# Kernel optimization log

Hardware: AMD Instinct MI355X
Metric: run time of the kernel (lower is better)

Reference implementation:

```python
import jax, jax.numpy as jnp
import numpy as np

B, N, D_SIM = 4096, 64, 768
NLI_DIM = 768
KK = 5
H1, NUM_CLASSES = 1024, 4


def setup_inputs() -> dict:
    key = jax.random.key(0)
    ks = jax.random.split(key, 8)
    sim_stance_emb = jax.random.normal(ks[0], (B, D_SIM), dtype=jnp.float32)
    nli_stance_emb = jax.random.normal(ks[1], (B, NLI_DIM), dtype=jnp.float32)
    sim_body_emb = jax.random.normal(ks[2], (B, N, D_SIM), dtype=jnp.float32)
    nli_body_emb = jax.random.normal(ks[3], (B, N, NLI_DIM), dtype=jnp.float32)
    fan1 = (KK + 1) * NLI_DIM
    W1 = jax.random.uniform(ks[4], (H1, fan1), jnp.float32, -1.0, 1.0) / jnp.sqrt(fan1)
    b1 = jax.random.uniform(ks[5], (H1,), jnp.float32, -1.0, 1.0) / jnp.sqrt(fan1)
    W2 = jax.random.uniform(ks[6], (NUM_CLASSES, H1), jnp.float32, -1.0, 1.0) / jnp.sqrt(H1)
    b2 = jax.random.uniform(ks[7], (NUM_CLASSES,), jnp.float32, -1.0, 1.0) / jnp.sqrt(H1)
    return {"sim_stance_emb": sim_stance_emb, "nli_stance_emb": nli_stance_emb,
            "sim_body_emb": sim_body_emb, "nli_body_emb": nli_body_emb,
            "W1": W1, "b1": b1, "W2": W2, "b2": b2}


def reference(sim_stance_emb, nli_stance_emb, sim_body_emb, nli_body_emb, W1, b1, W2, b2):
    # sims[b, n] = <sim_stance_emb[b], sim_body_emb[b, n]>  (bmm + squeeze)
    sims = jnp.einsum('bd,bnd->bn', sim_stance_emb, sim_body_emb)
    _, top_idx = jax.lax.top_k(sims, KK)                      # [B, KK]
    # gather top-k nli body sentence embeddings: [B, KK, NLI_DIM]
    top_emb = jnp.take_along_axis(nli_body_emb, top_idx[:, :, None], axis=1)
    xx = jnp.concatenate([nli_stance_emb, top_emb.reshape(top_emb.shape[0], -1)], axis=1)
    xx = jax.nn.relu(xx @ W1.T + b1)
    return xx @ W2.T + b2
```

## Files before the change

kernel.cpp:

```cpp
#include <hip/hip_runtime.h>
#include <stdint.h>
#include <stddef.h>

#define B_N   4096
#define NSENT 64
#define DDIM  768
#define TOPK  5
#define FAN1  4608
#define H1DIM 1024
#define NCLS  4
#define KDIM  4608

typedef __attribute__((ext_vector_type(8))) __bf16 bf16x8;
typedef __attribute__((ext_vector_type(4))) float  f32x4;

__device__ __forceinline__ unsigned short f2bf(float f) {
    unsigned int u = __float_as_uint(f);
    unsigned int r = (u + 0x7fffu + ((u >> 16) & 1u)) >> 16;
    return (unsigned short)r;
}

__device__ __forceinline__ void gl_lds16(const void* g, void* l) {
    __builtin_amdgcn_global_load_lds((__attribute__((address_space(1))) void*)(g),
                                     (__attribute__((address_space(3))) void*)(l),
                                     16, 0, 0);
}

__global__ __launch_bounds__(256) void k_topk_gather(
    const float* __restrict__ sim_stance,
    const float* __restrict__ sim_body,
    const float* __restrict__ nli_stance,
    const float* __restrict__ nli_body,
    unsigned short* __restrict__ xx)
{
    const int b    = blockIdx.x;
    const int tid  = threadIdx.x;
    const int lane = tid & 63;
    const int wave = tid >> 6;
    const int g    = lane >> 4;
    const int c    = lane & 15;
    __shared__ float sims[NSENT];
    __shared__ int   topidx[TOPK];

    const float4* st4 = (const float4*)(sim_stance + (size_t)b * DDIM);
    float4 st[12];
    #pragma unroll
    for (int j = 0; j < 12; ++j) st[j] = st4[c + 16 * j];

    const float* bodyb = sim_body + (size_t)b * NSENT * DDIM;
    #pragma unroll 1
    for (int it = 0; it < 4; ++it) {
        const int r = wave * 16 + it * 4 + g;
        const float4* r4 = (const float4*)(bodyb + (size_t)r * DDIM);
        float p = 0.f;
        #pragma unroll
        for (int j = 0; j < 12; ++j) {
            float4 v = r4[c + 16 * j];
            p += v.x*st[j].x + v.y*st[j].y + v.z*st[j].z + v.w*st[j].w;
        }
        #pragma unroll
        for (int off = 8; off; off >>= 1) p += __shfl_xor(p, off);
        if (c == 0) sims[r] = p;
    }
    __syncthreads();

    if (wave == 0) {
        float v = sims[lane];
        #pragma unroll
        for (int k = 0; k < TOPK; ++k) {
            float bv = v; int bi = lane;
            #pragma unroll
            for (int off = 32; off; off >>= 1) {
                float ov = __shfl_xor(bv, off);
                int   oi = __shfl_xor(bi, off);
                if (ov > bv || (ov == bv && oi < bi)) { bv = ov; bi = oi; }
            }
            if (lane == 0) topidx[k] = bi;
            if (lane == bi) v = -3.402823466e38f;
        }
    }
    __syncthreads();

    unsigned short* xrow = xx + (size_t)b * FAN1;
    for (int task = tid; task < 1152; task += 256) {
        const int seg = task / 192;
        const int t   = task - seg * 192;
        const float* src = (seg == 0)
            ? (nli_stance + (size_t)b * DDIM)
            : (nli_body + ((size_t)b * NSENT + topidx[seg - 1]) * DDIM);
        float4 v = ((const float4*)src)[t];
        ushort4 o;
        o.x = f2bf(v.x); o.y = f2bf(v.y); o.z = f2bf(v.z); o.w = f2bf(v.w);
        ((ushort4*)(xrow + seg * DDIM))[t] = o;
    }
}

__global__ __launch_bounds__(256) void k_f32_to_bf16x4(
    const float* __restrict__ in, unsigned short* __restrict__ o, int n4)
{
    int i = blockIdx.x * 256 + threadIdx.x;
    if (i < n4) {
        float4 v = ((const float4*)in)[i];
        ushort4 r;
        r.x = f2bf(v.x); r.y = f2bf(v.y); r.z = f2bf(v.z); r.w = f2bf(v.w);
        ((ushort4*)o)[i] = r;
    }
}

__global__ __launch_bounds__(256, 2) void k_gemm1(
    const unsigned short* __restrict__ A,
    const unsigned short* __restrict__ W,
    const float* __restrict__ bias,
    float* __restrict__ Hd)
{
    constexpr int BM = 128, BN = 64, BK = 64;
    constexpr int K = KDIM;
    __shared__ unsigned short lA[BM * BK];
    __shared__ unsigned short lB[BN * BK];

    const int tid = threadIdx.x, lane = tid & 63, wave = tid >> 6;
    const int bid = blockIdx.x;
    const int wk  = (bid & 7) * 64 + (bid >> 3);
    const int bn  = wk & 15, bm = wk >> 4;
    const int wm = wave >> 1, wn = wave & 1;

    const int q   = wave * 64 + lane;
    const int q8  = q >> 3;
    const int sc  = (q & 7) ^ (q8 & 7);
    const unsigned short* gA[4];
    const unsigned short* gB[2];
    #pragma unroll
    for (int j = 0; j < 4; ++j)
        gA[j] = A + (size_t)(bm * BM + j * 32 + q8) * K + sc * 8;
    #pragma unroll
    for (int j = 0; j < 2; ++j)
        gB[j] = W + (size_t)(bn * BN + j * 32 + q8) * K + sc * 8;
    unsigned short* lAd[4];
    unsigned short* lBd[2];
    #pragma unroll
    for (int j = 0; j < 4; ++j) lAd[j] = &lA[(j * 256 + wave * 64) * 8];
    #pragma unroll
    for (int j = 0; j < 2; ++j) lBd[j] = &lB[(j * 256 + wave * 64) * 8];

    const int r16 = lane & 15;
    const int p0  = (lane >> 4) ^ (r16 & 7);
    const int p1  = p0 ^ 4;
    const unsigned short* paBase = &lA[(wm * 64 + r16) * BK];
    const unsigned short* pbBase = &lB[(wn * 32 + r16) * BK];

    f32x4 acc[4][2];
    #pragma unroll
    for (int m = 0; m < 4; ++m)
        #pragma unroll
        for (int n = 0; n < 2; ++n) acc[m][n] = {0.f, 0.f, 0.f, 0.f};

    for (int kt = 0; kt < K / BK; ++kt) {
        #pragma unroll
        for (int j = 0; j < 4; ++j) { gl_lds16(gA[j], lAd[j]); gA[j] += BK; }
        #pragma unroll
        for (int j = 0; j < 2; ++j) { gl_lds16(gB[j], lBd[j]); gB[j] += BK; }
        __syncthreads();

        bf16x8 fa[4][2], fb[2][2];
        #pragma unroll
        for (int m = 0; m < 4; ++m) {
            fa[m][0] = *(const bf16x8*)(paBase + m * 16 * BK + p0 * 8);
            fa[m][1] = *(const bf16x8*)(paBase + m * 16 * BK + p1 * 8);
        }
        #pragma unroll
        for (int n = 0; n < 2; ++n) {
            fb[n][0] = *(const bf16x8*)(pbBase + n * 16 * BK + p0 * 8);
            fb[n][1] = *(const bf16x8*)(pbBase + n * 16 * BK + p1 * 8);
        }
        #pragma unroll
        for (int h = 0; h < 2; ++h)
            #pragma unroll
            for (int m = 0; m < 4; ++m)
                #pragma unroll
                for (int n = 0; n < 2; ++n)
                    acc[m][n] = __builtin_amdgcn_mfma_f32_16x16x32_bf16(
                        fa[m][h], fb[n][h], acc[m][n], 0, 0, 0);
        __syncthreads();
    }

    const int colbase = bn * BN + wn * 32 + r16;
    const int rowbase = bm * BM + wm * 64 + (lane >> 4) * 4;
    #pragma unroll
    for (int n = 0; n < 2; ++n) {
        const int col = colbase + n * 16;
        const float bv = bias[col];
        #pragma unroll
        for (int m = 0; m < 4; ++m) {
            const int row = rowbase + m * 16;
            #pragma unroll
            for (int j = 0; j < 4; ++j) {
                float v = acc[m][n][j] + bv;
                Hd[(size_t)(row + j) * H1DIM + col] = v > 0.f ? v : 0.f;
            }
        }
    }
}

__global__ __launch_bounds__(256) void k_gemm2(
    const float* __restrict__ Hd, const float* __restrict__ W2,
    const float* __restrict__ b2, float* __restrict__ out)
{
    __shared__ float w2s[NCLS * H1DIM];
    const int tid = threadIdx.x, lane = tid & 63, wave = tid >> 6;
    const int row = blockIdx.x * 4 + wave;
    for (int i = tid; i < NCLS * H1DIM; i += 256) w2s[i] = W2[i];
    __syncthreads();

    const float4* h4 = (const float4*)(Hd + (size_t)row * H1DIM);
    const float4* w0 = (const float4*)&w2s[0];
    const float4* w1 = (const float4*)&w2s[H1DIM];
    const float4* w2 = (const float4*)&w2s[2 * H1DIM];
    const float4* w3 = (const float4*)&w2s[3 * H1DIM];
    float a0 = 0.f, a1 = 0.f, a2 = 0.f, a3 = 0.f;
    #pragma unroll
    for (int j = 0; j < 4; ++j) {
        const int idx = j * 64 + lane;
        float4 h = h4[idx], xv;
        xv = w0[idx]; a0 += h.x*xv.x + h.y*xv.y + h.z*xv.z + h.w*xv.w;
        xv = w1[idx]; a1 += h.x*xv.x + h.y*xv.y + h.z*xv.z + h.w*xv.w;
        xv = w2[idx]; a2 += h.x*xv.x + h.y*xv.y + h.z*xv.z + h.w*xv.w;
        xv = w3[idx]; a3 += h.x*xv.x + h.y*xv.y + h.z*xv.z + h.w*xv.w;
    }
    #pragma unroll
    for (int off = 32; off; off >>= 1) {
        a0 += __shfl_xor(a0, off);
        a1 += __shfl_xor(a1, off);
        a2 += __shfl_xor(a2, off);
        a3 += __shfl_xor(a3, off);
    }
    if (lane == 0) {
        float* o = out + (size_t)row * NCLS;
        o[0] = a0 + b2[0]; o[1] = a1 + b2[1]; o[2] = a2 + b2[2]; o[3] = a3 + b2[3];
    }
}

extern "C" void kernel_launch(void* const* d_in, const int* in_sizes, int n_in,
                              void* d_out, int out_size, void* d_ws, size_t ws_size,
                              hipStream_t stream)
{
    const float* sim_stance = (const float*)d_in[0];
    const float* nli_stance = (const float*)d_in[1];
    const float* sim_body   = (const float*)d_in[2];
    const float* nli_body   = (const float*)d_in[3];
    const float* W1 = (const float*)d_in[4];
    const float* b1 = (const float*)d_in[5];
    const float* W2 = (const float*)d_in[6];
    const float* b2 = (const float*)d_in[7];
    float* out = (float*)d_out;

    char* ws = (char*)d_ws;
    unsigned short* xx     = (unsigned short*)ws;
    unsigned short* w1b    = (unsigned short*)(ws + 37748736u);
    float*          hidden = (float*)(ws + 37748736u + 9437184u);

    k_f32_to_bf16x4<<<dim3(4608), dim3(256), 0, stream>>>(W1, w1b, 1179648);
    k_topk_gather<<<dim3(B_N), dim3(256), 0, stream>>>(sim_stance, sim_body,
                                                       nli_stance, nli_body, xx);
    k_gemm1<<<dim3(512), dim3(256), 0, stream>>>(xx, w1b, b1, hidden);
    k_gemm2<<<dim3(1024), dim3(256), 0, stream>>>(hidden, W2, b2, out);
}
```

Measured before the change: 274.5 us.

## Use 128x128 GEMM1 tiles with split-K of two, reducing partials in GEMM2

GEMM1 now uses 128x128 output tiles and splits K into two halves, so 512 blocks still fill the GPU while each block has higher arithmetic intensity and reuses operands more. Each half writes fp32 partial sums to a workspace. GEMM2 then adds the two partials and the bias, applies ReLU, and does the final projection. This lowers global-to-LDS traffic per FLOP and raises MFMA work per block. In exchange it doubles the fp32 hidden-activation traffic, writing and reading two 16 MB partial buffers, and uses more accumulator registers.

```diff
diff --git a/kernel.cpp b/kernel.cpp
--- a/kernel.cpp
+++ b/kernel.cpp
@@ -10,6 +10,7 @@
 #define H1DIM 1024
 #define NCLS  4
 #define KDIM  4608
+#define KHALF 2304
 
 typedef __attribute__((ext_vector_type(8))) __bf16 bf16x8;
 typedef __attribute__((ext_vector_type(4))) float  f32x4;
@@ -110,10 +111,9 @@
 __global__ __launch_bounds__(256, 2) void k_gemm1(
     const unsigned short* __restrict__ A,
     const unsigned short* __restrict__ W,
-    const float* __restrict__ bias,
-    float* __restrict__ Hd)
-{
-    constexpr int BM = 128, BN = 64, BK = 64;
+    float* __restrict__ P)
+{
+    constexpr int BM = 128, BN = 128, BK = 64;
     constexpr int K = KDIM;
     __shared__ unsigned short lA[BM * BK];
     __shared__ unsigned short lB[BN * BK];
@@ -121,54 +121,56 @@
     const int tid = threadIdx.x, lane = tid & 63, wave = tid >> 6;
     const int bid = blockIdx.x;
     const int wk  = (bid & 7) * 64 + (bid >> 3);
-    const int bn  = wk & 15, bm = wk >> 4;
+    const int ks  = wk >> 8;
+    const int rem = wk & 255;
+    const int bm  = rem >> 3, bn = rem & 7;
     const int wm = wave >> 1, wn = wave & 1;
-
-    const int q   = wave * 64 + lane;
-    const int q8  = q >> 3;
-    const int sc  = (q & 7) ^ (q8 & 7);
+    const int k0 = ks * KHALF;
+
+    const int rowq = wave * 8 + (lane >> 3);
+    const int sc   = (lane & 7) ^ (lane >> 3);
     const unsigned short* gA[4];
-    const unsigned short* gB[2];
-    #pragma unroll
-    for (int j = 0; j < 4; ++j)
-        gA[j] = A + (size_t)(bm * BM + j * 32 + q8) * K + sc * 8;
-    #pragma unroll
-    for (int j = 0; j < 2; ++j)
-        gB[j] = W + (size_t)(bn * BN + j * 32 + q8) * K + sc * 8;
+    const unsigned short* gB[4];
+    #pragma unroll
+    for (int j = 0; j < 4; ++j) {
+        gA[j] = A + (size_t)(bm * BM + j * 32 + rowq) * K + k0 + sc * 8;
+        gB[j] = W + (size_t)(bn * BN + j * 32 + rowq) * K + k0 + sc * 8;
+    }
     unsigned short* lAd[4];
-    unsigned short* lBd[2];
-    #pragma unroll
-    for (int j = 0; j < 4; ++j) lAd[j] = &lA[(j * 256 + wave * 64) * 8];
-    #pragma unroll
-    for (int j = 0; j < 2; ++j) lBd[j] = &lB[(j * 256 + wave * 64) * 8];
+    unsigned short* lBd[4];
+    #pragma unroll
+    for (int j = 0; j < 4; ++j) {
+        lAd[j] = &lA[(j * 256 + wave * 64) * 8];
+        lBd[j] = &lB[(j * 256 + wave * 64) * 8];
+    }
 
     const int r16 = lane & 15;
     const int p0  = (lane >> 4) ^ (r16 & 7);
     const int p1  = p0 ^ 4;
     const unsigned short* paBase = &lA[(wm * 64 + r16) * BK];
-    const unsigned short* pbBase = &lB[(wn * 32 + r16) * BK];
-
-    f32x4 acc[4][2];
+    const unsigned short* pbBase = &lB[(wn * 64 + r16) * BK];
+
+    f32x4 acc[4][4];
     #pragma unroll
     for (int m = 0; m < 4; ++m)
         #pragma unroll
-        for (int n = 0; n < 2; ++n) acc[m][n] = {0.f, 0.f, 0.f, 0.f};
-
-    for (int kt = 0; kt < K / BK; ++kt) {
+        for (int n = 0; n < 4; ++n) acc[m][n] = {0.f, 0.f, 0.f, 0.f};
+
+    for (int kt = 0; kt < KHALF / BK; ++kt) {
         #pragma unroll
         for (int j = 0; j < 4; ++j) { gl_lds16(gA[j], lAd[j]); gA[j] += BK; }
         #pragma unroll
-        for (int j = 0; j < 2; ++j) { gl_lds16(gB[j], lBd[j]); gB[j] += BK; }
+        for (int j = 0; j < 4; ++j) { gl_lds16(gB[j], lBd[j]); gB[j] += BK; }
         __syncthreads();
 
-        bf16x8 fa[4][2], fb[2][2];
+        bf16x8 fa[4][2], fb[4][2];
         #pragma unroll
         for (int m = 0; m < 4; ++m) {
             fa[m][0] = *(const bf16x8*)(paBase + m * 16 * BK + p0 * 8);
             fa[m][1] = *(const bf16x8*)(paBase + m * 16 * BK + p1 * 8);
         }
         #pragma unroll
-        for (int n = 0; n < 2; ++n) {
+        for (int n = 0; n < 4; ++n) {
             fb[n][0] = *(const bf16x8*)(pbBase + n * 16 * BK + p0 * 8);
             fb[n][1] = *(const bf16x8*)(pbBase + n * 16 * BK + p1 * 8);
         }
@@ -177,50 +179,58 @@
             #pragma unroll
             for (int m = 0; m < 4; ++m)
                 #pragma unroll
-                for (int n = 0; n < 2; ++n)
+                for (int n = 0; n < 4; ++n)
                     acc[m][n] = __builtin_amdgcn_mfma_f32_16x16x32_bf16(
                         fa[m][h], fb[n][h], acc[m][n], 0, 0, 0);
         __syncthreads();
     }
 
-    const int colbase = bn * BN + wn * 32 + r16;
+    float* Pk = P + (size_t)ks * B_N * H1DIM;
+    const int colbase = bn * BN + wn * 64 + r16;
     const int rowbase = bm * BM + wm * 64 + (lane >> 4) * 4;
     #pragma unroll
-    for (int n = 0; n < 2; ++n) {
+    for (int n = 0; n < 4; ++n) {
         const int col = colbase + n * 16;
-        const float bv = bias[col];
         #pragma unroll
         for (int m = 0; m < 4; ++m) {
             const int row = rowbase + m * 16;
             #pragma unroll
-            for (int j = 0; j < 4; ++j) {
-                float v = acc[m][n][j] + bv;
-                Hd[(size_t)(row + j) * H1DIM + col] = v > 0.f ? v : 0.f;
-            }
+            for (int j = 0; j < 4; ++j)
+                Pk[(size_t)(row + j) * H1DIM + col] = acc[m][n][j];
         }
     }
 }
 
 __global__ __launch_bounds__(256) void k_gemm2(
-    const float* __restrict__ Hd, const float* __restrict__ W2,
-    const float* __restrict__ b2, float* __restrict__ out)
-{
-    __shared__ float w2s[NCLS * H1DIM];
+    const float* __restrict__ P, const float* __restrict__ W2,
+    const float* __restrict__ b1, const float* __restrict__ b2,
+    float* __restrict__ out)
+{
+    __shared__ float w2s[NCLS * H1DIM + H1DIM];
     const int tid = threadIdx.x, lane = tid & 63, wave = tid >> 6;
     const int row = blockIdx.x * 4 + wave;
     for (int i = tid; i < NCLS * H1DIM; i += 256) w2s[i] = W2[i];
+    for (int i = tid; i < H1DIM; i += 256) w2s[NCLS * H1DIM + i] = b1[i];
     __syncthreads();
 
-    const float4* h4 = (const float4*)(Hd + (size_t)row * H1DIM);
+    const float4* p0 = (const float4*)(P + (size_t)row * H1DIM);
+    const float4* p1 = (const float4*)(P + (size_t)(B_N + row) * H1DIM);
     const float4* w0 = (const float4*)&w2s[0];
     const float4* w1 = (const float4*)&w2s[H1DIM];
     const float4* w2 = (const float4*)&w2s[2 * H1DIM];
     const float4* w3 = (const float4*)&w2s[3 * H1DIM];
+    const float4* bb = (const float4*)&w2s[4 * H1DIM];
     float a0 = 0.f, a1 = 0.f, a2 = 0.f, a3 = 0.f;
     #pragma unroll
     for (int j = 0; j < 4; ++j) {
         const int idx = j * 64 + lane;
-        float4 h = h4[idx], xv;
+        float4 x0 = p0[idx], x1 = p1[idx], bv = bb[idx];
+        float4 h;
+        h.x = x0.x + x1.x + bv.x; h.x = h.x > 0.f ? h.x : 0.f;
+        h.y = x0.y + x1.y + bv.y; h.y = h.y > 0.f ? h.y : 0.f;
+        h.z = x0.z + x1.z + bv.z; h.z = h.z > 0.f ? h.z : 0.f;
+        h.w = x0.w + x1.w + bv.w; h.w = h.w > 0.f ? h.w : 0.f;
+        float4 xv;
         xv = w0[idx]; a0 += h.x*xv.x + h.y*xv.y + h.z*xv.z + h.w*xv.w;
         xv = w1[idx]; a1 += h.x*xv.x + h.y*xv.y + h.z*xv.z + h.w*xv.w;
         xv = w2[idx]; a2 += h.x*xv.x + h.y*xv.y + h.z*xv.z + h.w*xv.w;
@@ -254,13 +264,13 @@
     float* out = (float*)d_out;
 
     char* ws = (char*)d_ws;
-    unsigned short* xx     = (unsigned short*)ws;
-    unsigned short* w1b    = (unsigned short*)(ws + 37748736u);
-    float*          hidden = (float*)(ws + 37748736u + 9437184u);
+    unsigned short* xx  = (unsigned short*)ws;
+    unsigned short* w1b = (unsigned short*)(ws + 37748736u);
+    float*          P   = (float*)(ws + 37748736u + 9437184u);
 
     k_f32_to_bf16x4<<<dim3(4608), dim3(256), 0, stream>>>(W1, w1b, 1179648);
     k_topk_gather<<<dim3(B_N), dim3(256), 0, stream>>>(sim_stance, sim_body,
                                                        nli_stance, nli_body, xx);
-    k_gemm1<<<dim3(512), dim3(256), 0, stream>>>(xx, w1b, b1, hidden);
-    k_gemm2<<<dim3(1024), dim3(256), 0, stream>>>(hidden, W2, b2, out);
-}
+    k_gemm1<<<dim3(512), dim3(256), 0, stream>>>(xx, w1b, P);
+    k_gemm2<<<dim3(1024), dim3(256), 0, stream>>>(P, W2, b1, b2, out);
+}
```

Measured after the change: 255.0 us. 1.08x faster.
